# Kernel optimization log

Measured on AMD Instinct MI355X. Metric: run time of the kernel, lower is better.

Reference implementation:

```python
import jax, jax.numpy as jnp
import numpy as np

WINDOW = 7
NUM_NODES = 20000
IN_CH = 8
HID = 64
N_TOTAL = WINDOW * NUM_NODES          # 140000 supra-nodes (window x nodes)
N_EDGES = N_TOTAL * 16                # avg degree 16
EPS = 1e-5                            # BatchNorm1d eps


def setup_inputs() -> dict:
    key = jax.random.key(0)
    ks = jax.random.split(key, 12)
    return {
        "_x": jax.random.normal(ks[0], (N_TOTAL, IN_CH), jnp.float32),
        "edge_idx": jax.random.randint(ks[1], (2, N_EDGES), 0, N_TOTAL, dtype=jnp.int32),
        "edge_wgt": jax.random.uniform(ks[2], (N_EDGES,), jnp.float32),
        # GCNConv 1 / 2 (weight stored as [in, out])
        "W1": jax.random.normal(ks[3], (IN_CH, HID), jnp.float32) / np.sqrt(IN_CH).astype(np.float32),
        "b1": jnp.zeros((HID,), jnp.float32),
        "W2": jax.random.normal(ks[4], (HID, HID), jnp.float32) / np.sqrt(HID).astype(np.float32),
        "b2": jnp.zeros((HID,), jnp.float32),
        # BatchNorm1d 1 / 2
        "gamma1": jnp.ones((HID,), jnp.float32),
        "beta1": jnp.zeros((HID,), jnp.float32),
        "gamma2": jnp.ones((HID,), jnp.float32),
        "beta2": jnp.zeros((HID,), jnp.float32),
        # LSTM 1: input 2*HID -> HID ; LSTM 2: HID -> HID (PyTorch gate order i,f,g,o)
        "Wih1": jax.random.normal(ks[5], (4 * HID, 2 * HID), jnp.float32) / np.sqrt(2 * HID).astype(np.float32),
        "Whh1": jax.random.normal(ks[6], (4 * HID, HID), jnp.float32) / np.sqrt(HID).astype(np.float32),
        "bih1": jnp.zeros((4 * HID,), jnp.float32),
        "bhh1": jnp.zeros((4 * HID,), jnp.float32),
        "Wih2": jax.random.normal(ks[7], (4 * HID, HID), jnp.float32) / np.sqrt(HID).astype(np.float32),
        "Whh2": jax.random.normal(ks[8], (4 * HID, HID), jnp.float32) / np.sqrt(HID).astype(np.float32),
        "bih2": jnp.zeros((4 * HID,), jnp.float32),
        "bhh2": jnp.zeros((4 * HID,), jnp.float32),
    }


def _batch_norm(x, gamma, beta):
    # training-mode BatchNorm1d: batch statistics, biased variance
    m = x.mean(axis=0)
    v = ((x - m) ** 2).mean(axis=0)
    return (x - m) * jax.lax.rsqrt(v + EPS) * gamma + beta


def _lstm(seq, Wih, Whh, bih, bhh):
    # seq: [T, B, D]; PyTorch gate order (i, f, g, o); zero initial state
    B = seq.shape[1]
    H = Whh.shape[1]
    h0 = jnp.zeros((B, H), seq.dtype)

    def step(carry, xt):
        h, c = carry
        gates = xt @ Wih.T + h @ Whh.T + bih + bhh   # [B, 4H]
        i, f, g, o = jnp.split(gates, 4, axis=1)
        c = jax.nn.sigmoid(f) * c + jax.nn.sigmoid(i) * jnp.tanh(g)
        h = jax.nn.sigmoid(o) * jnp.tanh(c)
        return (h, c), h

    (hT, _), ys = jax.lax.scan(step, (h0, h0), seq)
    return ys, hT


def _forward(_x, edge_idx, edge_wgt, W1, b1, W2, b2, gamma1, beta1, gamma2, beta2,
             Wih1, Whh1, bih1, bhh1, Wih2, Whh2, bih2, bhh2):
    # --- skip connection S: [num_nodes, in_ch + window - 1] ---
    S = _x.reshape(-1, WINDOW, NUM_NODES, IN_CH).transpose(0, 2, 1, 3).reshape(-1, WINDOW, IN_CH)
    S = jnp.concatenate([S[:, 0, :], S[:, 1:, IN_CH - 1]], axis=1)

    # --- symmetric GCN normalization with self loops (gcn_norm, fill=1.0) ---
    loop = jnp.arange(N_TOTAL, dtype=edge_idx.dtype)
    src = jnp.concatenate([edge_idx[0], loop])
    dst = jnp.concatenate([edge_idx[1], loop])
    w = jnp.concatenate([edge_wgt, jnp.ones((N_TOTAL,), edge_wgt.dtype)])
    deg = jax.ops.segment_sum(w, dst, num_segments=N_TOTAL)
    dinv = jnp.where(deg > 0, jax.lax.rsqrt(jnp.where(deg > 0, deg, 1.0)), 0.0)
    norm = dinv[src] * w * dinv[dst]  # [E+N]

    def gconv(h, W, b):
        msg = (h @ W)[src] * norm[:, None]                     # gather + scale
        return jax.ops.segment_sum(msg, dst, num_segments=N_TOTAL) + b  # scatter-add

    # dropout is identity in eval mode (deterministic baseline)
    X1 = _batch_norm(jax.nn.relu(gconv(_x, W1, b1)), gamma1, beta1)
    X2 = _batch_norm(jax.nn.relu(gconv(X1, W2, b2)), gamma2, beta2)

    Xc = jnp.concatenate([X1, X2], axis=1)                     # [window*nodes, 2H]
    Xc = Xc.reshape(-1, WINDOW, NUM_NODES, 2 * HID).transpose(1, 0, 2, 3)
    Xc = Xc.reshape(WINDOW, -1, 2 * HID)                       # [T, B*nodes, 2H]

    ys1, H1 = _lstm(Xc, Wih1, Whh1, bih1, bhh1)
    _, H2 = _lstm(ys1, Wih2, Whh2, bih2, bhh2)

    return jnp.concatenate([H1, H2, S], axis=1)  # [nodes, 2H + in_ch + window - 1]


def reference(_x, edge_idx, edge_wgt, W1, b1, W2, b2, gamma1, beta1, gamma2, beta2,
              Wih1, Whh1, bih1, bhh1, Wih2, Whh2, bih2, bhh2):
    return _forward(_x, edge_idx, edge_wgt, W1, b1, W2, b2, gamma1, beta1, gamma2, beta2,
                    Wih1, Whh1, bih1, bhh1, Wih2, Whh2, bih2, bhh2)
```

## Files before the change

### kernel.cpp

```cpp
#include <hip/hip_runtime.h>


#define N_TOT 140000
#define NQUAD 35000
#define NE    2240000
#define NODES 20000
#define TWIN  7
#define CIN   8
#define HD    64
#define OUTC  142
#define SLOTS 48
#define WQ    16383.0f
#define NPART 8
#define PSIZE 17500
#define NTILES 1250
#define HTILES 8750

typedef __attribute__((ext_vector_type(8))) short short8;
typedef __attribute__((ext_vector_type(4))) float f32x4;

static __device__ __forceinline__ float fast_exp2(float x) {
  return __builtin_amdgcn_exp2f(x);
}
static __device__ __forceinline__ float fast_rcp(float x) {
  return __builtin_amdgcn_rcpf(x);
}
static __device__ __forceinline__ float sigf(float x) {
  return fast_rcp(1.0f + fast_exp2(-1.4426950408889634f * x));
}
static __device__ __forceinline__ float tanhf_(float x) {
  return 1.0f - 2.0f * fast_rcp(1.0f + fast_exp2(2.8853900817779268f * x));
}
static __device__ __forceinline__ ushort f2bf(float x) {
  union { float f; uint32_t u; } c; c.f = x;
  uint32_t r = c.u + 0x7fff + ((c.u >> 16) & 1);
  return (ushort)(r >> 16);
}
static __device__ __forceinline__ float bf2f(ushort h) {
  union { uint32_t u; float f; } c; c.u = ((uint32_t)h) << 16; return c.f;
}
static __device__ __forceinline__ float wdec(uint v) {
  return (float)(v & 16383u) * (1.0f / WQ);
}

__global__ __launch_bounds__(256) void k_wpack0(const float* __restrict__ Whh1,
                                                const float* __restrict__ Wih2,
                                                const float* __restrict__ Whh2,
                                                const float* __restrict__ bih2,
                                                const float* __restrict__ bhh2,
                                                ushort* __restrict__ Wphh1,
                                                ushort* __restrict__ Wpih2,
                                                ushort* __restrict__ Wphh2,
                                                float* __restrict__ bsum2) {
  int b = blockIdx.x;
  if (b < 192) {
    int which = b >> 6;
    int idx = (b & 63) * 256 + threadIdx.x;
    const float* W = (which == 0) ? Whh1 : (which == 1) ? Wih2 : Whh2;
    ushort* Wp = (which == 0) ? Wphh1 : (which == 1) ? Wpih2 : Wphh2;
    int j = idx & 7, lane = (idx >> 3) & 63, nt = (idx >> 9) & 15, kc = idx >> 13;
    int g = nt * 16 + (lane & 15);
    int k = kc * 32 + ((lane >> 4) << 3) + j;
    Wp[idx] = f2bf(W[g * 64 + k]);
  } else {
    bsum2[threadIdx.x] = bih2[threadIdx.x] + bhh2[threadIdx.x];
  }
}

__global__ __launch_bounds__(256) void k_mid1(const float* __restrict__ W2,
                                              const float* __restrict__ scale1,
                                              const float* __restrict__ shift1,
                                              ushort* __restrict__ Wp2,
                                              float* __restrict__ c2b) {
  int b = blockIdx.x;
  if (b < 16) {
    int idx = b * 256 + threadIdx.x;
    int jj = idx & 7, lane = (idx >> 3) & 63, nt = (idx >> 9) & 3, kc = idx >> 11;
    int j = nt * 16 + (lane & 15);
    int k = kc * 32 + ((lane >> 4) << 3) + jj;
    Wp2[idx] = f2bf(scale1[k] * W2[k * 64 + j]);
  } else if (threadIdx.x < HD) {
    int j = threadIdx.x;
    float s = 0.f;
    for (int k = 0; k < HD; ++k) s += shift1[k] * W2[k * 64 + j];
    c2b[j] = s;
  }
}

__global__ __launch_bounds__(256) void k_mid2(const float* __restrict__ Wih1,
                                              const float* __restrict__ scale1,
                                              const float* __restrict__ scale2,
                                              const float* __restrict__ shift1,
                                              const float* __restrict__ shift2,
                                              const float* __restrict__ bih1,
                                              const float* __restrict__ bhh1,
                                              ushort* __restrict__ Wp1,
                                              float* __restrict__ biasL1) {
  int b = blockIdx.x;
  if (b < 128) {
    int idx = b * 256 + threadIdx.x;
    int j = idx & 7, lane = (idx >> 3) & 63, nt = (idx >> 9) & 15, kc = idx >> 13;
    int g = nt * 16 + (lane & 15);
    int k = kc * 32 + ((lane >> 4) << 3) + j;
    float s = (k < HD) ? scale1[k] : scale2[k - HD];
    Wp1[idx] = f2bf(Wih1[g * 128 + k] * s);
  } else {
    int col = threadIdx.x;
    float s = bih1[col] + bhh1[col];
    for (int k = 0; k < HD; ++k) s += Wih1[col * 128 + k] * shift1[k];
    for (int k = 0; k < HD; ++k) s += Wih1[col * 128 + HD + k] * shift2[k];
    biasL1[col] = s;
  }
}

__global__ __launch_bounds__(256) void k_fill_part(const int* __restrict__ srcI,
                                                   const int* __restrict__ dstI,
                                                   const float* __restrict__ w,
                                                   int* cursor,
                                                   uint* __restrict__ csr) {
  int b = blockIdx.x;
  int part = b & (NPART - 1);
  int chunk = b >> 3;
  int nchunks = gridDim.x >> 3;
  int per = (NE + nchunks - 1) / nchunks;
  int lo = chunk * per;
  int hi = min(lo + per, NE);
  int plo = part * PSIZE;
  for (int e = lo + threadIdx.x; e < hi; e += 256) {
    int d = dstI[e];
    unsigned du = (unsigned)(d - plo);
    if (du < (unsigned)PSIZE) {
      int s = srcI[e];
      float wv = w[e];
      int pos = atomicAdd(&cursor[d], 1);
      if (pos < SLOTS) {
        uint q = (uint)(wv * WQ + 0.5f);
        csr[(size_t)d * SLOTS + pos] = ((uint)s << 14) | q;
      }
    }
  }
}

__global__ __launch_bounds__(256) void k_prep4(const int* __restrict__ cursor,
                                               uint* __restrict__ csr,
                                               const float* __restrict__ x,
                                               float* __restrict__ dinv,
                                               ushort* __restrict__ xs) {
  int wv = (blockIdx.x * 256 + threadIdx.x) >> 6;
  int lane = threadIdx.x & 63;
  int nw = (gridDim.x * 256) >> 6;
  for (int p = wv; p < NQUAD; p += nw) {
    int d0 = p * 4;
    int len[4];
    float ws[4];
    #pragma unroll
    for (int r = 0; r < 4; ++r) {
      len[r] = min(cursor[d0 + r], SLOTS);
      ws[r] = (lane < len[r]) ? wdec(csr[(size_t)(d0 + r) * SLOTS + lane]) : 0.f;
    }
    #pragma unroll
    for (int m = 1; m < 64; m <<= 1) {
      #pragma unroll
      for (int r = 0; r < 4; ++r) ws[r] += __shfl_xor(ws[r], m);
    }
    float di[4];
    #pragma unroll
    for (int r = 0; r < 4; ++r) di[r] = rsqrtf(1.0f + ws[r]);
    if (lane < 4) dinv[d0 + lane] = di[lane];
    int lenM = (max(max(len[0], len[1]), max(len[2], len[3])) + 7) & ~7;
    #pragma unroll
    for (int r = 0; r < 4; ++r)
      if (lane >= len[r] && lane < lenM) csr[(size_t)(d0 + r) * SLOTS + lane] = 0u;
    if (lane < 4 * CIN) {
      int r = lane >> 3, c = lane & 7;
      xs[(size_t)(d0 + r) * CIN + c] = f2bf(di[r] * x[(size_t)(d0 + r) * CIN + c]);
    }
  }
}

__global__ __launch_bounds__(256) void k_gcn1(const ushort* __restrict__ xs,
                                              const float* __restrict__ dinv,
                                              const int* __restrict__ cursor,
                                              const uint* __restrict__ csr,
                                              const float* __restrict__ W1,
                                              const float* __restrict__ b1,
                                              ushort* __restrict__ A1,
                                              float* gsum, float* gsq) {
  __shared__ float w1s[CIN * HD];
  __shared__ float b1s[HD];
  for (int i = threadIdx.x; i < CIN * HD; i += 256) w1s[i] = W1[i];
  if (threadIdx.x < HD) b1s[threadIdx.x] = b1[threadIdx.x];
  __syncthreads();
  int wv = (blockIdx.x * 256 + threadIdx.x) >> 6;
  int lane = threadIdx.x & 63;
  int nw = (gridDim.x * 256) >> 6;
  int e8 = lane >> 3, c8 = lane & 7;
  float s = 0.f, q = 0.f;
  for (int p = wv; p < NQUAD; p += nw) {
    int d0 = p * 4;
    const uint* row0 = csr + (size_t)(d0 + 0) * SLOTS;
    const uint* row1 = csr + (size_t)(d0 + 1) * SLOTS;
    const uint* row2 = csr + (size_t)(d0 + 2) * SLOTS;
    const uint* row3 = csr + (size_t)(d0 + 3) * SLOTS;
    int l0 = min(cursor[d0 + 0], SLOTS), l1 = min(cursor[d0 + 1], SLOTS);
    int l2 = min(cursor[d0 + 2], SLOTS), l3 = min(cursor[d0 + 3], SLOTS);
    int lenM = (max(max(l0, l1), max(l2, l3)) + 7) & ~7;
    float p0 = 0.f, p1 = 0.f, p2 = 0.f, p3 = 0.f;
    #pragma unroll 2
    for (int i = e8; i < lenM; i += 8) {
      uint c0 = row0[i], c1 = row1[i], c2 = row2[i], c3 = row3[i];
      p0 += wdec(c0) * bf2f(xs[(size_t)(c0 >> 14) * CIN + c8]);
      p1 += wdec(c1) * bf2f(xs[(size_t)(c1 >> 14) * CIN + c8]);
      p2 += wdec(c2) * bf2f(xs[(size_t)(c2 >> 14) * CIN + c8]);
      p3 += wdec(c3) * bf2f(xs[(size_t)(c3 >> 14) * CIN + c8]);
    }
    #pragma unroll
    for (int m = 8; m < 64; m <<= 1) {
      p0 += __shfl_xor(p0, m); p1 += __shfl_xor(p1, m);
      p2 += __shfl_xor(p2, m); p3 += __shfl_xor(p3, m);
    }
    p0 += bf2f(xs[(size_t)(d0 + 0) * CIN + c8]);
    p1 += bf2f(xs[(size_t)(d0 + 1) * CIN + c8]);
    p2 += bf2f(xs[(size_t)(d0 + 2) * CIN + c8]);
    p3 += bf2f(xs[(size_t)(d0 + 3) * CIN + c8]);
    float di0 = dinv[d0 + 0], di1 = dinv[d0 + 1];
    float di2 = dinv[d0 + 2], di3 = dinv[d0 + 3];
    float a0 = b1s[lane], a1 = b1s[lane], a2 = b1s[lane], a3 = b1s[lane];
    #pragma unroll
    for (int c = 0; c < CIN; ++c) {
      float wgt = w1s[c * HD + lane];
      a0 += di0 * __shfl(p0, c) * wgt;
      a1 += di1 * __shfl(p1, c) * wgt;
      a2 += di2 * __shfl(p2, c) * wgt;
      a3 += di3 * __shfl(p3, c) * wgt;
    }
    float r0 = fmaxf(a0, 0.f), r1 = fmaxf(a1, 0.f);
    float r2 = fmaxf(a2, 0.f), r3 = fmaxf(a3, 0.f);
    A1[(size_t)(d0 + 0) * HD + lane] = f2bf(r0);
    A1[(size_t)(d0 + 1) * HD + lane] = f2bf(r1);
    A1[(size_t)(d0 + 2) * HD + lane] = f2bf(r2);
    A1[(size_t)(d0 + 3) * HD + lane] = f2bf(r3);
    s += r0 + r1 + r2 + r3;
    q += r0 * r0 + r1 * r1 + r2 * r2 + r3 * r3;
  }
  atomicAdd(&gsum[lane], s);
  atomicAdd(&gsq[lane], q);
}

__global__ __launch_bounds__(64) void k_bnfin(const float* __restrict__ gsum,
                                              const float* __restrict__ gsq,
                                              const float* __restrict__ gamma,
                                              const float* __restrict__ beta,
                                              float* __restrict__ scale,
                                              float* __restrict__ shift) {
  int j = threadIdx.x;
  if (j < HD) {
    float m = gsum[j] / (float)N_TOT;
    float v = gsq[j] / (float)N_TOT - m * m;
    float sc = gamma[j] * rsqrtf(v + 1e-5f);
    scale[j] = sc;
    shift[j] = beta[j] - m * sc;
  }
}

__global__ __launch_bounds__(256) void k_gemm_h2(const ushort* __restrict__ A1,
                                                 const ushort* __restrict__ Wp2,
                                                 const float* __restrict__ c2b,
                                                 const float* __restrict__ dinv,
                                                 ushort* __restrict__ Hbs) {
  int t = threadIdx.x, wid = t >> 6, lane = t & 63;
  int tile = blockIdx.x * 4 + wid;
  if (tile >= HTILES) return;
  int g = lane >> 4, c = lane & 15;
  const ushort* ap = A1 + ((size_t)(tile * 16 + c)) * HD + g * 8;
  f32x4 acc[4];
  #pragma unroll
  for (int nt = 0; nt < 4; ++nt) {
    float bv = c2b[nt * 16 + c];
    acc[nt] = (f32x4){bv, bv, bv, bv};
  }
  #pragma unroll
  for (int kc = 0; kc < 2; ++kc) {
    short8 a = *reinterpret_cast<const short8*>(ap + kc * 32);
    #pragma unroll
    for (int nt = 0; nt < 4; ++nt) {
      short8 b = *reinterpret_cast<const short8*>(&Wp2[((kc * 4 + nt) * 64 + lane) * 8]);
      acc[nt] = __builtin_amdgcn_mfma_f32_16x16x32_bf16(a, b, acc[nt], 0, 0, 0);
    }
  }
  float dv[4];
  #pragma unroll
  for (int jr = 0; jr < 4; ++jr) dv[jr] = dinv[tile * 16 + g * 4 + jr];
  #pragma unroll
  for (int nt = 0; nt < 4; ++nt)
    #pragma unroll
    for (int jr = 0; jr < 4; ++jr) {
      int r = g * 4 + jr;
      Hbs[((size_t)(tile * 16 + r)) * HD + nt * 16 + c] = f2bf(dv[jr] * acc[nt][jr]);
    }
}

__global__ __launch_bounds__(256) void k_spmm2(const ushort* __restrict__ Hbs,
                                               const float* __restrict__ dinv,
                                               const int* __restrict__ cursor,
                                               const uint* __restrict__ csr,
                                               const float* __restrict__ bias,
                                               ushort* __restrict__ A2,
                                               float* gsum, float* gsq) {
  int wv = (blockIdx.x * 256 + threadIdx.x) >> 6;
  int lane = threadIdx.x & 63;
  int nw = (gridDim.x * 256) >> 6;
  float b = bias[lane];
  float s = 0.f, q = 0.f;
  for (int p = wv; p < NQUAD; p += nw) {
    int d0 = p * 4;
    const uint* row0 = csr + (size_t)(d0 + 0) * SLOTS;
    const uint* row1 = csr + (size_t)(d0 + 1) * SLOTS;
    const uint* row2 = csr + (size_t)(d0 + 2) * SLOTS;
    const uint* row3 = csr + (size_t)(d0 + 3) * SLOTS;
    int l0 = min(cursor[d0 + 0], SLOTS), l1 = min(cursor[d0 + 1], SLOTS);
    int l2 = min(cursor[d0 + 2], SLOTS), l3 = min(cursor[d0 + 3], SLOTS);
    int lenM = (max(max(l0, l1), max(l2, l3)) + 7) & ~7;
    float a0 = bf2f(Hbs[(size_t)(d0 + 0) * HD + lane]);
    float a1 = bf2f(Hbs[(size_t)(d0 + 1) * HD + lane]);
    float a2 = bf2f(Hbs[(size_t)(d0 + 2) * HD + lane]);
    float a3 = bf2f(Hbs[(size_t)(d0 + 3) * HD + lane]);
    for (int i0 = 0; i0 < lenM; i0 += 8) {
      uint cv0[8], cv1[8], cv2[8], cv3[8];
      #pragma unroll
      for (int j = 0; j < 8; ++j) {
        cv0[j] = row0[i0 + j]; cv1[j] = row1[i0 + j];
        cv2[j] = row2[i0 + j]; cv3[j] = row3[i0 + j];
      }
      ushort h0[8], h1[8], h2[8], h3[8];
      #pragma unroll
      for (int j = 0; j < 8; ++j) {
        h0[j] = Hbs[((size_t)(cv0[j] >> 14)) * HD + lane];
        h1[j] = Hbs[((size_t)(cv1[j] >> 14)) * HD + lane];
        h2[j] = Hbs[((size_t)(cv2[j] >> 14)) * HD + lane];
        h3[j] = Hbs[((size_t)(cv3[j] >> 14)) * HD + lane];
      }
      #pragma unroll
      for (int j = 0; j < 8; ++j) {
        a0 = fmaf(wdec(cv0[j]), bf2f(h0[j]), a0);
        a1 = fmaf(wdec(cv1[j]), bf2f(h1[j]), a1);
        a2 = fmaf(wdec(cv2[j]), bf2f(h2[j]), a2);
        a3 = fmaf(wdec(cv3[j]), bf2f(h3[j]), a3);
      }
    }
    float r0 = fmaxf(dinv[d0 + 0] * a0 + b, 0.f);
    float r1 = fmaxf(dinv[d0 + 1] * a1 + b, 0.f);
    float r2 = fmaxf(dinv[d0 + 2] * a2 + b, 0.f);
    float r3 = fmaxf(dinv[d0 + 3] * a3 + b, 0.f);
    A2[(size_t)(d0 + 0) * HD + lane] = f2bf(r0);
    A2[(size_t)(d0 + 1) * HD + lane] = f2bf(r1);
    A2[(size_t)(d0 + 2) * HD + lane] = f2bf(r2);
    A2[(size_t)(d0 + 3) * HD + lane] = f2bf(r3);
    s += r0 + r1 + r2 + r3;
    q += r0 * r0 + r1 * r1 + r2 * r2 + r3 * r3;
  }
  atomicAdd(&gsum[lane], s);
  atomicAdd(&gsq[lane], q);
}

__global__ __launch_bounds__(256) void k_lstm5(const ushort* __restrict__ A1,
                                               const ushort* __restrict__ A2,
                                               const ushort* __restrict__ Wp1,
                                               const ushort* __restrict__ Wphh1,
                                               const ushort* __restrict__ Wpih2,
                                               const ushort* __restrict__ Wphh2,
                                               const float* __restrict__ biasL1,
                                               const float* __restrict__ bsum2,
                                               const float* __restrict__ x,
                                               float* __restrict__ out) {
  __shared__ ushort h1s[2][1024];
  __shared__ ushort h2s[2][1024];
  int t = threadIdx.x;
  int q = t >> 6, lane = t & 63;
  int tile = blockIdx.x;
  int g = lane >> 4, c = lane & 15;

  float c1[4], c2[4];
  #pragma unroll
  for (int i = 0; i < 4; ++i) { c1[i] = 0.f; c2[i] = 0.f; }

  int hr[2];
  #pragma unroll
  for (int kc = 0; kc < 2; ++kc)
    hr[kc] = (c * 64 + kc * 32 + g * 8) ^ ((c & 7) << 3);
  int hw[4];
  #pragma unroll
  for (int jr = 0; jr < 4; ++jr) {
    int r = g * 4 + jr, j = q * 16 + c;
    hw[jr] = (r * 64 + j) ^ ((r & 7) << 3);
  }
  float bL1[4], bL2[4];
  #pragma unroll
  for (int gi = 0; gi < 4; ++gi) {
    bL1[gi] = biasL1[gi * 64 + q * 16 + c];
    bL2[gi] = bsum2[gi * 64 + q * 16 + c];
  }

  for (int step = 0; step < TWIN; ++step) {
    int pw = step & 1, pr = pw ^ 1;
    size_t nodeoff = (size_t)(step * NODES + tile * 16 + c) * HD + g * 8;
    const ushort* a1p = A1 + nodeoff;
    const ushort* a2p = A2 + nodeoff;

    f32x4 acc[4];
    #pragma unroll
    for (int gi = 0; gi < 4; ++gi) acc[gi] = (f32x4){bL1[gi], bL1[gi], bL1[gi], bL1[gi]};
    #pragma unroll
    for (int kc = 0; kc < 4; ++kc) {
      const ushort* ap = (kc < 2) ? (a1p + kc * 32) : (a2p + (kc - 2) * 32);
      short8 a = *reinterpret_cast<const short8*>(ap);
      #pragma unroll
      for (int gi = 0; gi < 4; ++gi) {
        short8 b = *reinterpret_cast<const short8*>(&Wp1[((kc * 16 + gi * 4 + q) * 64 + lane) * 8]);
        acc[gi] = __builtin_amdgcn_mfma_f32_16x16x32_bf16(a, b, acc[gi], 0, 0, 0);
      }
    }
    if (step > 0) {
      #pragma unroll
      for (int kc = 0; kc < 2; ++kc) {
        short8 a = *reinterpret_cast<const short8*>(&h1s[pr][hr[kc]]);
        #pragma unroll
        for (int gi = 0; gi < 4; ++gi) {
          short8 b = *reinterpret_cast<const short8*>(&Wphh1[((kc * 16 + gi * 4 + q) * 64 + lane) * 8]);
          acc[gi] = __builtin_amdgcn_mfma_f32_16x16x32_bf16(a, b, acc[gi], 0, 0, 0);
        }
      }
    }
    #pragma unroll
    for (int jr = 0; jr < 4; ++jr) {
      float gi_ = acc[0][jr], gf = acc[1][jr], gg = acc[2][jr], go = acc[3][jr];
      float cc = sigf(gf) * c1[jr] + sigf(gi_) * tanhf_(gg);
      c1[jr] = cc;
      float h = sigf(go) * tanhf_(cc);
      h1s[pw][hw[jr]] = f2bf(h);
      if (step == TWIN - 1) {
        int r = g * 4 + jr, j = q * 16 + c;
        out[(size_t)(tile * 16 + r) * OUTC + j] = h;
      }
    }
    __syncthreads();

    #pragma unroll
    for (int gi = 0; gi < 4; ++gi) acc[gi] = (f32x4){bL2[gi], bL2[gi], bL2[gi], bL2[gi]};
    #pragma unroll
    for (int kc = 0; kc < 2; ++kc) {
      short8 a = *reinterpret_cast<const short8*>(&h1s[pw][hr[kc]]);
      #pragma unroll
      for (int gi = 0; gi < 4; ++gi) {
        short8 b = *reinterpret_cast<const short8*>(&Wpih2[((kc * 16 + gi * 4 + q) * 64 + lane) * 8]);
        acc[gi] = __builtin_amdgcn_mfma_f32_16x16x32_bf16(a, b, acc[gi], 0, 0, 0);
      }
    }
    if (step > 0) {
      #pragma unroll
      for (int kc = 0; kc < 2; ++kc) {
        short8 a = *reinterpret_cast<const short8*>(&h2s[pr][hr[kc]]);
        #pragma unroll
        for (int gi = 0; gi < 4; ++gi) {
          short8 b = *reinterpret_cast<const short8*>(&Wphh2[((kc * 16 + gi * 4 + q) * 64 + lane) * 8]);
          acc[gi] = __builtin_amdgcn_mfma_f32_16x16x32_bf16(a, b, acc[gi], 0, 0, 0);
        }
      }
    }
    #pragma unroll
    for (int jr = 0; jr < 4; ++jr) {
      float gi_ = acc[0][jr], gf = acc[1][jr], gg = acc[2][jr], go = acc[3][jr];
      float cc = sigf(gf) * c2[jr] + sigf(gi_) * tanhf_(gg);
      c2[jr] = cc;
      float h = sigf(go) * tanhf_(cc);
      h2s[pw][hw[jr]] = f2bf(h);
      if (step == TWIN - 1) {
        int r = g * 4 + jr, j = q * 16 + c;
        out[(size_t)(tile * 16 + r) * OUTC + HD + j] = h;
      }
    }
    __syncthreads();
  }

  for (int idx = t; idx < 16 * 14; idx += 256) {
    int r = idx / 14, cc = idx - r * 14;
    int n = tile * 16 + r;
    float v = (cc < CIN) ? x[(size_t)n * CIN + cc]
                         : x[((size_t)(cc - (CIN - 1)) * NODES + n) * CIN + (CIN - 1)];
    out[(size_t)n * OUTC + 128 + cc] = v;
  }
}

extern "C" void kernel_launch(void* const* d_in, const int* in_sizes, int n_in,
                              void* d_out, int out_size, void* d_ws, size_t ws_size,
                              hipStream_t stream) {
  const float* x      = (const float*)d_in[0];
  const int*   ei     = (const int*)d_in[1];
  const float* ew     = (const float*)d_in[2];
  const float* W1     = (const float*)d_in[3];
  const float* b1     = (const float*)d_in[4];
  const float* W2     = (const float*)d_in[5];
  const float* b2     = (const float*)d_in[6];
  const float* gamma1 = (const float*)d_in[7];
  const float* beta1  = (const float*)d_in[8];
  const float* gamma2 = (const float*)d_in[9];
  const float* beta2  = (const float*)d_in[10];
  const float* Wih1   = (const float*)d_in[11];
  const float* Whh1   = (const float*)d_in[12];
  const float* bih1   = (const float*)d_in[13];
  const float* bhh1   = (const float*)d_in[14];
  const float* Wih2   = (const float*)d_in[15];
  const float* Whh2   = (const float*)d_in[16];
  const float* bih2   = (const float*)d_in[17];
  const float* bhh2   = (const float*)d_in[18];
  const int* srcI = ei;
  const int* dstI = ei + NE;
  float* out = (float*)d_out;

  char* base = (char*)d_ws;
  size_t off = 0;
  auto alloc = [&](size_t bytes) -> void* {
    void* p = base + off;
    off = (off + bytes + 255) & ~(size_t)255;
    return p;
  };
  float* dinv   = (float*)alloc(N_TOT * 4);
  ushort* xs    = (ushort*)alloc((size_t)N_TOT * CIN * 2);
  ushort* Wp1   = (ushort*)alloc(32768 * 2);
  ushort* Wphh1 = (ushort*)alloc(16384 * 2);
  ushort* Wpih2 = (ushort*)alloc(16384 * 2);
  ushort* Wphh2 = (ushort*)alloc(16384 * 2);
  ushort* Wp2   = (ushort*)alloc(4096 * 2);
  float* c2b    = (float*)alloc(HD * 4);
  float* biasL1 = (float*)alloc(256 * 4);
  float* bsum2  = (float*)alloc(256 * 4);
  float* scale1 = (float*)alloc(HD * 4);
  float* shift1 = (float*)alloc(HD * 4);
  float* scale2 = (float*)alloc(HD * 4);
  float* shift2 = (float*)alloc(HD * 4);
  char* zstart = base + off;
  int*   cursor = (int*)alloc(N_TOT * 4);
  float* sum1   = (float*)alloc(HD * 4);
  float* sq1    = (float*)alloc(HD * 4);
  float* sum2   = (float*)alloc(HD * 4);
  float* sq2    = (float*)alloc(HD * 4);
  size_t zbytes = (size_t)((base + off) - zstart);
  uint*   csr = (uint*)alloc((size_t)N_TOT * SLOTS * 4);
  ushort* Hbs = (ushort*)alloc((size_t)N_TOT * HD * 2);
  ushort* A1  = (ushort*)alloc((size_t)N_TOT * HD * 2);
  ushort* A2  = (ushort*)alloc((size_t)N_TOT * HD * 2);

  hipMemsetAsync(zstart, 0, zbytes, stream);
  k_wpack0<<<193, 256, 0, stream>>>(Whh1, Wih2, Whh2, bih2, bhh2,
                                    Wphh1, Wpih2, Wphh2, bsum2);
  k_fill_part<<<1024, 256, 0, stream>>>(srcI, dstI, ew, cursor, csr);
  k_prep4<<<1024, 256, 0, stream>>>(cursor, csr, x, dinv, xs);
  k_gcn1<<<1024, 256, 0, stream>>>(xs, dinv, cursor, csr, W1, b1, A1, sum1, sq1);
  k_bnfin<<<1, 64, 0, stream>>>(sum1, sq1, gamma1, beta1, scale1, shift1);
  k_mid1<<<17, 256, 0, stream>>>(W2, scale1, shift1, Wp2, c2b);
  k_gemm_h2<<<(HTILES + 3) / 4, 256, 0, stream>>>(A1, Wp2, c2b, dinv, Hbs);
  k_spmm2<<<1024, 256, 0, stream>>>(Hbs, dinv, cursor, csr, b2, A2, sum2, sq2);
  k_bnfin<<<1, 64, 0, stream>>>(sum2, sq2, gamma2, beta2, scale2, shift2);
  k_mid2<<<129, 256, 0, stream>>>(Wih1, scale1, scale2, shift1, shift2,
                                  bih1, bhh1, Wp1, biasL1);
  k_lstm5<<<NTILES, 256, 0, stream>>>(A1, A2, Wp1, Wphh1, Wpih2, Wphh2,
                                      biasL1, bsum2, x, out);
}
```

Before: 521.9 us.

## Replace partitioned edge scan with two-pass binning before CSR fill

Before, the CSR fill had each of the 8 partitions re-read the whole edge list (src, dst, weight) and keep only its destination range, so edge reads were repeated 8 times. Now one pass stages edges in shared memory and scatters packed (dst, src|weight) records into per-partition global bins. A second kernel fills CSR slots from each bin. This cuts repeated global reads but adds an extra kernel launch, a round trip of about 18MB of binned records, and a fixed bin capacity that can overflow if the destinations are skewed.

```diff
diff --git a/kernel.cpp b/kernel.cpp
--- a/kernel.cpp
+++ b/kernel.cpp
@@ -13,6 +13,7 @@
 #define WQ    16383.0f
 #define NPART 8
 #define PSIZE 17500
+#define BCAP  290816
 #define NTILES 1250
 #define HTILES 8750
 
@@ -113,31 +114,63 @@
   }
 }
 
-__global__ __launch_bounds__(256) void k_fill_part(const int* __restrict__ srcI,
-                                                   const int* __restrict__ dstI,
-                                                   const float* __restrict__ w,
-                                                   int* cursor,
-                                                   uint* __restrict__ csr) {
+__global__ __launch_bounds__(256) void k_bin(const int* __restrict__ srcI,
+                                             const int* __restrict__ dstI,
+                                             const float* __restrict__ w,
+                                             int* binCnt,
+                                             uint2* __restrict__ binBuf) {
+  __shared__ uint2 stage[NPART][256];
+  __shared__ int scnt[NPART];
+  __shared__ int sbase[NPART];
+  int tid = threadIdx.x;
+  int per = (NE + gridDim.x - 1) / gridDim.x;
+  int lo = blockIdx.x * per;
+  int hi = min(lo + per, NE);
+  if (tid < NPART) scnt[tid] = 0;
+  __syncthreads();
+  for (int e0 = lo; e0 < hi; e0 += 256) {
+    int e = e0 + tid;
+    if (e < hi) {
+      int d = dstI[e];
+      int s = srcI[e];
+      float wv = w[e];
+      int part = d / PSIZE;
+      uint packed = ((uint)s << 14) | (uint)(wv * WQ + 0.5f);
+      int pos = atomicAdd(&scnt[part], 1);
+      stage[part][pos] = make_uint2((uint)d, packed);
+    }
+    __syncthreads();
+    int bin = tid >> 5, ln = tid & 31;
+    if (ln == 0) sbase[bin] = atomicAdd(&binCnt[bin], scnt[bin]);
+    __syncthreads();
+    int n = scnt[bin];
+    size_t base = (size_t)bin * BCAP + sbase[bin];
+    for (int i = ln; i < n; i += 32)
+      binBuf[base + i] = stage[bin][i];
+    __syncthreads();
+    if (tid < NPART) scnt[tid] = 0;
+    __syncthreads();
+  }
+}
+
+__global__ __launch_bounds__(256) void k_fill_p2(const int* __restrict__ binCnt,
+                                                 const uint2* __restrict__ binBuf,
+                                                 int* cursor,
+                                                 uint* __restrict__ csr) {
   int b = blockIdx.x;
   int part = b & (NPART - 1);
   int chunk = b >> 3;
-  int nchunks = gridDim.x >> 3;
-  int per = (NE + nchunks - 1) / nchunks;
+  int nch = gridDim.x >> 3;
+  int cnt = binCnt[part];
+  int per = (cnt + nch - 1) / nch;
   int lo = chunk * per;
-  int hi = min(lo + per, NE);
-  int plo = part * PSIZE;
-  for (int e = lo + threadIdx.x; e < hi; e += 256) {
-    int d = dstI[e];
-    unsigned du = (unsigned)(d - plo);
-    if (du < (unsigned)PSIZE) {
-      int s = srcI[e];
-      float wv = w[e];
-      int pos = atomicAdd(&cursor[d], 1);
-      if (pos < SLOTS) {
-        uint q = (uint)(wv * WQ + 0.5f);
-        csr[(size_t)d * SLOTS + pos] = ((uint)s << 14) | q;
-      }
-    }
+  int hi = min(lo + per, cnt);
+  const uint2* buf = binBuf + (size_t)part * BCAP;
+  for (int i = lo + threadIdx.x; i < hi; i += 256) {
+    uint2 rec = buf[i];
+    int d = (int)rec.x;
+    int pos = atomicAdd(&cursor[d], 1);
+    if (pos < SLOTS) csr[(size_t)d * SLOTS + pos] = rec.y;
   }
 }
 
@@ -540,12 +573,14 @@
   float* shift2 = (float*)alloc(HD * 4);
   char* zstart = base + off;
   int*   cursor = (int*)alloc(N_TOT * 4);
+  int*   binCnt = (int*)alloc(NPART * 4);
   float* sum1   = (float*)alloc(HD * 4);
   float* sq1    = (float*)alloc(HD * 4);
   float* sum2   = (float*)alloc(HD * 4);
   float* sq2    = (float*)alloc(HD * 4);
   size_t zbytes = (size_t)((base + off) - zstart);
-  uint*   csr = (uint*)alloc((size_t)N_TOT * SLOTS * 4);
+  uint*   csr    = (uint*)alloc((size_t)N_TOT * SLOTS * 4);
+  uint2*  binBuf = (uint2*)alloc((size_t)NPART * BCAP * 8);
   ushort* Hbs = (ushort*)alloc((size_t)N_TOT * HD * 2);
   ushort* A1  = (ushort*)alloc((size_t)N_TOT * HD * 2);
   ushort* A2  = (ushort*)alloc((size_t)N_TOT * HD * 2);
@@ -553,7 +588,8 @@
   hipMemsetAsync(zstart, 0, zbytes, stream);
   k_wpack0<<<193, 256, 0, stream>>>(Whh1, Wih2, Whh2, bih2, bhh2,
                                     Wphh1, Wpih2, Wphh2, bsum2);
-  k_fill_part<<<1024, 256, 0, stream>>>(srcI, dstI, ew, cursor, csr);
+  k_bin<<<1024, 256, 0, stream>>>(srcI, dstI, ew, binCnt, binBuf);
+  k_fill_p2<<<1024, 256, 0, stream>>>(binCnt, binBuf, cursor, csr);
   k_prep4<<<1024, 256, 0, stream>>>(cursor, csr, x, dinv, xs);
   k_gcn1<<<1024, 256, 0, stream>>>(xs, dinv, cursor, csr, W1, b1, A1, sum1, sq1);
   k_bnfin<<<1, 64, 0, stream>>>(sum1, sq1, gamma1, beta1, scale1, shift1);
```

Result: slower. 939.1 us (+80.0%).

## Split padded CSR into 16-slot primary array plus 32-slot overflow array

Applied to the files above, without the earlier changes.

The padded adjacency of 48 slots per node becomes a dense 16-slot primary array and a separate 32-slot overflow array. The first 16 neighbours are always processed with a fully unrolled fixed loop, and the overflow is read only when a quad of nodes has more than 16 edges. The goal is denser, better-cached edge-list reads, since most nodes (average degree 16) fit in the primary block. The cost is extra branching and a second pass over overflow rows for the roughly half of quads with higher-degree nodes, and the fixed loop always reads all 16 primary slots even for short rows.

```diff
diff --git a/kernel.cpp b/kernel.cpp
--- a/kernel.cpp
+++ b/kernel.cpp
@@ -117,7 +117,8 @@
                                                    const int* __restrict__ dstI,
                                                    const float* __restrict__ w,
                                                    int* cursor,
-                                                   uint* __restrict__ csr) {
+                                                   uint* __restrict__ csr16,
+                                                   uint* __restrict__ csrOvf) {
   int b = blockIdx.x;
   int part = b & (NPART - 1);
   int chunk = b >> 3;
@@ -133,22 +134,23 @@
       int s = srcI[e];
       float wv = w[e];
       int pos = atomicAdd(&cursor[d], 1);
-      if (pos < SLOTS) {
-        uint q = (uint)(wv * WQ + 0.5f);
-        csr[(size_t)d * SLOTS + pos] = ((uint)s << 14) | q;
-      }
+      uint packed = ((uint)s << 14) | (uint)(wv * WQ + 0.5f);
+      if (pos < 16)         csr16[(size_t)d * 16 + pos] = packed;
+      else if (pos < SLOTS) csrOvf[(size_t)d * 32 + (pos - 16)] = packed;
     }
   }
 }
 
 __global__ __launch_bounds__(256) void k_prep4(const int* __restrict__ cursor,
-                                               uint* __restrict__ csr,
+                                               uint* __restrict__ csr16,
+                                               uint* __restrict__ csrOvf,
                                                const float* __restrict__ x,
                                                float* __restrict__ dinv,
                                                ushort* __restrict__ xs) {
   int wv = (blockIdx.x * 256 + threadIdx.x) >> 6;
   int lane = threadIdx.x & 63;
   int nw = (gridDim.x * 256) >> 6;
+  int sl = lane - 16;
   for (int p = wv; p < NQUAD; p += nw) {
     int d0 = p * 4;
     int len[4];
@@ -156,7 +158,13 @@
     #pragma unroll
     for (int r = 0; r < 4; ++r) {
       len[r] = min(cursor[d0 + r], SLOTS);
-      ws[r] = (lane < len[r]) ? wdec(csr[(size_t)(d0 + r) * SLOTS + lane]) : 0.f;
+      float v = 0.f;
+      if (lane < 16) {
+        if (lane < len[r]) v = wdec(csr16[(size_t)(d0 + r) * 16 + lane]);
+      } else if (lane < 48) {
+        if (sl < len[r] - 16) v = wdec(csrOvf[(size_t)(d0 + r) * 32 + sl]);
+      }
+      ws[r] = v;
     }
     #pragma unroll
     for (int m = 1; m < 64; m <<= 1) {
@@ -167,10 +175,15 @@
     #pragma unroll
     for (int r = 0; r < 4; ++r) di[r] = rsqrtf(1.0f + ws[r]);
     if (lane < 4) dinv[d0 + lane] = di[lane];
-    int lenM = (max(max(len[0], len[1]), max(len[2], len[3])) + 7) & ~7;
-    #pragma unroll
-    for (int r = 0; r < 4; ++r)
-      if (lane >= len[r] && lane < lenM) csr[(size_t)(d0 + r) * SLOTS + lane] = 0u;
+    int mo = max(max(len[0], len[1]), max(len[2], len[3])) - 16;
+    int ovfM = (mo > 0) ? ((mo + 7) & ~7) : 0;
+    #pragma unroll
+    for (int r = 0; r < 4; ++r) {
+      if (lane < 16 && lane >= len[r]) csr16[(size_t)(d0 + r) * 16 + lane] = 0u;
+      int ovfLen = max(len[r] - 16, 0);
+      if (lane >= 16 && sl >= ovfLen && sl < ovfM)
+        csrOvf[(size_t)(d0 + r) * 32 + sl] = 0u;
+    }
     if (lane < 4 * CIN) {
       int r = lane >> 3, c = lane & 7;
       xs[(size_t)(d0 + r) * CIN + c] = f2bf(di[r] * x[(size_t)(d0 + r) * CIN + c]);
@@ -181,7 +194,8 @@
 __global__ __launch_bounds__(256) void k_gcn1(const ushort* __restrict__ xs,
                                               const float* __restrict__ dinv,
                                               const int* __restrict__ cursor,
-                                              const uint* __restrict__ csr,
+                                              const uint* __restrict__ csr16,
+                                              const uint* __restrict__ csrOvf,
                                               const float* __restrict__ W1,
                                               const float* __restrict__ b1,
                                               ushort* __restrict__ A1,
@@ -198,21 +212,36 @@
   float s = 0.f, q = 0.f;
   for (int p = wv; p < NQUAD; p += nw) {
     int d0 = p * 4;
-    const uint* row0 = csr + (size_t)(d0 + 0) * SLOTS;
-    const uint* row1 = csr + (size_t)(d0 + 1) * SLOTS;
-    const uint* row2 = csr + (size_t)(d0 + 2) * SLOTS;
-    const uint* row3 = csr + (size_t)(d0 + 3) * SLOTS;
+    const uint* p0r = csr16 + (size_t)(d0 + 0) * 16;
+    const uint* p1r = csr16 + (size_t)(d0 + 1) * 16;
+    const uint* p2r = csr16 + (size_t)(d0 + 2) * 16;
+    const uint* p3r = csr16 + (size_t)(d0 + 3) * 16;
     int l0 = min(cursor[d0 + 0], SLOTS), l1 = min(cursor[d0 + 1], SLOTS);
     int l2 = min(cursor[d0 + 2], SLOTS), l3 = min(cursor[d0 + 3], SLOTS);
-    int lenM = (max(max(l0, l1), max(l2, l3)) + 7) & ~7;
     float p0 = 0.f, p1 = 0.f, p2 = 0.f, p3 = 0.f;
-    #pragma unroll 2
-    for (int i = e8; i < lenM; i += 8) {
-      uint c0 = row0[i], c1 = row1[i], c2 = row2[i], c3 = row3[i];
+    #pragma unroll
+    for (int ii = 0; ii < 2; ++ii) {
+      int i = ii * 8 + e8;
+      uint c0 = p0r[i], c1 = p1r[i], c2 = p2r[i], c3 = p3r[i];
       p0 += wdec(c0) * bf2f(xs[(size_t)(c0 >> 14) * CIN + c8]);
       p1 += wdec(c1) * bf2f(xs[(size_t)(c1 >> 14) * CIN + c8]);
       p2 += wdec(c2) * bf2f(xs[(size_t)(c2 >> 14) * CIN + c8]);
       p3 += wdec(c3) * bf2f(xs[(size_t)(c3 >> 14) * CIN + c8]);
+    }
+    int mo = max(max(l0, l1), max(l2, l3)) - 16;
+    int ovfM = (mo > 0) ? ((mo + 7) & ~7) : 0;
+    if (ovfM > 0) {
+      const uint* o0 = csrOvf + (size_t)(d0 + 0) * 32;
+      const uint* o1 = csrOvf + (size_t)(d0 + 1) * 32;
+      const uint* o2 = csrOvf + (size_t)(d0 + 2) * 32;
+      const uint* o3 = csrOvf + (size_t)(d0 + 3) * 32;
+      for (int i = e8; i < ovfM; i += 8) {
+        uint c0 = o0[i], c1 = o1[i], c2 = o2[i], c3 = o3[i];
+        p0 += wdec(c0) * bf2f(xs[(size_t)(c0 >> 14) * CIN + c8]);
+        p1 += wdec(c1) * bf2f(xs[(size_t)(c1 >> 14) * CIN + c8]);
+        p2 += wdec(c2) * bf2f(xs[(size_t)(c2 >> 14) * CIN + c8]);
+        p3 += wdec(c3) * bf2f(xs[(size_t)(c3 >> 14) * CIN + c8]);
+      }
     }
     #pragma unroll
     for (int m = 8; m < 64; m <<= 1) {
@@ -303,7 +332,8 @@
 __global__ __launch_bounds__(256) void k_spmm2(const ushort* __restrict__ Hbs,
                                                const float* __restrict__ dinv,
                                                const int* __restrict__ cursor,
-                                               const uint* __restrict__ csr,
+                                               const uint* __restrict__ csr16,
+                                               const uint* __restrict__ csrOvf,
                                                const float* __restrict__ bias,
                                                ushort* __restrict__ A2,
                                                float* gsum, float* gsq) {
@@ -314,23 +344,23 @@
   float s = 0.f, q = 0.f;
   for (int p = wv; p < NQUAD; p += nw) {
     int d0 = p * 4;
-    const uint* row0 = csr + (size_t)(d0 + 0) * SLOTS;
-    const uint* row1 = csr + (size_t)(d0 + 1) * SLOTS;
-    const uint* row2 = csr + (size_t)(d0 + 2) * SLOTS;
-    const uint* row3 = csr + (size_t)(d0 + 3) * SLOTS;
+    const uint* p0r = csr16 + (size_t)(d0 + 0) * 16;
+    const uint* p1r = csr16 + (size_t)(d0 + 1) * 16;
+    const uint* p2r = csr16 + (size_t)(d0 + 2) * 16;
+    const uint* p3r = csr16 + (size_t)(d0 + 3) * 16;
     int l0 = min(cursor[d0 + 0], SLOTS), l1 = min(cursor[d0 + 1], SLOTS);
     int l2 = min(cursor[d0 + 2], SLOTS), l3 = min(cursor[d0 + 3], SLOTS);
-    int lenM = (max(max(l0, l1), max(l2, l3)) + 7) & ~7;
     float a0 = bf2f(Hbs[(size_t)(d0 + 0) * HD + lane]);
     float a1 = bf2f(Hbs[(size_t)(d0 + 1) * HD + lane]);
     float a2 = bf2f(Hbs[(size_t)(d0 + 2) * HD + lane]);
     float a3 = bf2f(Hbs[(size_t)(d0 + 3) * HD + lane]);
-    for (int i0 = 0; i0 < lenM; i0 += 8) {
+    #pragma unroll
+    for (int i0 = 0; i0 < 16; i0 += 8) {
       uint cv0[8], cv1[8], cv2[8], cv3[8];
       #pragma unroll
       for (int j = 0; j < 8; ++j) {
-        cv0[j] = row0[i0 + j]; cv1[j] = row1[i0 + j];
-        cv2[j] = row2[i0 + j]; cv3[j] = row3[i0 + j];
+        cv0[j] = p0r[i0 + j]; cv1[j] = p1r[i0 + j];
+        cv2[j] = p2r[i0 + j]; cv3[j] = p3r[i0 + j];
       }
       ushort h0[8], h1[8], h2[8], h3[8];
       #pragma unroll
@@ -346,6 +376,37 @@
         a1 = fmaf(wdec(cv1[j]), bf2f(h1[j]), a1);
         a2 = fmaf(wdec(cv2[j]), bf2f(h2[j]), a2);
         a3 = fmaf(wdec(cv3[j]), bf2f(h3[j]), a3);
+      }
+    }
+    int mo = max(max(l0, l1), max(l2, l3)) - 16;
+    int ovfM = (mo > 0) ? ((mo + 7) & ~7) : 0;
+    if (ovfM > 0) {
+      const uint* o0 = csrOvf + (size_t)(d0 + 0) * 32;
+      const uint* o1 = csrOvf + (size_t)(d0 + 1) * 32;
+      const uint* o2 = csrOvf + (size_t)(d0 + 2) * 32;
+      const uint* o3 = csrOvf + (size_t)(d0 + 3) * 32;
+      for (int i0 = 0; i0 < ovfM; i0 += 8) {
+        uint cv0[8], cv1[8], cv2[8], cv3[8];
+        #pragma unroll
+        for (int j = 0; j < 8; ++j) {
+          cv0[j] = o0[i0 + j]; cv1[j] = o1[i0 + j];
+          cv2[j] = o2[i0 + j]; cv3[j] = o3[i0 + j];
+        }
+        ushort h0[8], h1[8], h2[8], h3[8];
+        #pragma unroll
+        for (int j = 0; j < 8; ++j) {
+          h0[j] = Hbs[((size_t)(cv0[j] >> 14)) * HD + lane];
+          h1[j] = Hbs[((size_t)(cv1[j] >> 14)) * HD + lane];
+          h2[j] = Hbs[((size_t)(cv2[j] >> 14)) * HD + lane];
+          h3[j] = Hbs[((size_t)(cv3[j] >> 14)) * HD + lane];
+        }
+        #pragma unroll
+        for (int j = 0; j < 8; ++j) {
+          a0 = fmaf(wdec(cv0[j]), bf2f(h0[j]), a0);
+          a1 = fmaf(wdec(cv1[j]), bf2f(h1[j]), a1);
+          a2 = fmaf(wdec(cv2[j]), bf2f(h2[j]), a2);
+          a3 = fmaf(wdec(cv3[j]), bf2f(h3[j]), a3);
+        }
       }
     }
     float r0 = fmaxf(dinv[d0 + 0] * a0 + b, 0.f);
@@ -545,7 +606,8 @@
   float* sum2   = (float*)alloc(HD * 4);
   float* sq2    = (float*)alloc(HD * 4);
   size_t zbytes = (size_t)((base + off) - zstart);
-  uint*   csr = (uint*)alloc((size_t)N_TOT * SLOTS * 4);
+  uint*   csr16  = (uint*)alloc((size_t)N_TOT * 16 * 4);
+  uint*   csrOvf = (uint*)alloc((size_t)N_TOT * 32 * 4);
   ushort* Hbs = (ushort*)alloc((size_t)N_TOT * HD * 2);
   ushort* A1  = (ushort*)alloc((size_t)N_TOT * HD * 2);
   ushort* A2  = (ushort*)alloc((size_t)N_TOT * HD * 2);
@@ -553,13 +615,13 @@
   hipMemsetAsync(zstart, 0, zbytes, stream);
   k_wpack0<<<193, 256, 0, stream>>>(Whh1, Wih2, Whh2, bih2, bhh2,
                                     Wphh1, Wpih2, Wphh2, bsum2);
-  k_fill_part<<<1024, 256, 0, stream>>>(srcI, dstI, ew, cursor, csr);
-  k_prep4<<<1024, 256, 0, stream>>>(cursor, csr, x, dinv, xs);
-  k_gcn1<<<1024, 256, 0, stream>>>(xs, dinv, cursor, csr, W1, b1, A1, sum1, sq1);
+  k_fill_part<<<1024, 256, 0, stream>>>(srcI, dstI, ew, cursor, csr16, csrOvf);
+  k_prep4<<<1024, 256, 0, stream>>>(cursor, csr16, csrOvf, x, dinv, xs);
+  k_gcn1<<<1024, 256, 0, stream>>>(xs, dinv, cursor, csr16, csrOvf, W1, b1, A1, sum1, sq1);
   k_bnfin<<<1, 64, 0, stream>>>(sum1, sq1, gamma1, beta1, scale1, shift1);
   k_mid1<<<17, 256, 0, stream>>>(W2, scale1, shift1, Wp2, c2b);
   k_gemm_h2<<<(HTILES + 3) / 4, 256, 0, stream>>>(A1, Wp2, c2b, dinv, Hbs);
-  k_spmm2<<<1024, 256, 0, stream>>>(Hbs, dinv, cursor, csr, b2, A2, sum2, sq2);
+  k_spmm2<<<1024, 256, 0, stream>>>(Hbs, dinv, cursor, csr16, csrOvf, b2, A2, sum2, sq2);
   k_bnfin<<<1, 64, 0, stream>>>(sum2, sq2, gamma2, beta2, scale2, shift2);
   k_mid2<<<129, 256, 0, stream>>>(Wih1, scale1, scale2, shift1, shift2,
                                   bih1, bhh1, Wp1, biasL1);
```

New measurement: 517.7 us, median of 2. Within noise of the previous version (-0.8%).
